# Optimization experiments

Measured on AMD Instinct MI355X. Metric: run time of the kernel, lower is better.

Reference implementation:

```python
import jax, jax.numpy as jnp
import numpy as np

N_NODES = 20000
N_EDGES = 320000
F_IN = 64      # num_node_features
C = 64         # out_features (per-head channels, concat=False)
H = 4          # n_heads
L = 3          # n_layers (stackable since F_IN == C)
N_RES = 2
N_PAIRS = 8192
EDGE_DIM = 9
HID = 64 * C   # ResNetGated hidden dim = 64 * out_features
N_EXPERTS = 8


def setup_inputs() -> dict:
    key = jax.random.key(0)
    ks = jax.random.split(key, 24)
    s = 0.05
    f32 = jnp.float32
    inp = {}
    inp["x"] = jax.random.normal(ks[0], (N_NODES, F_IN), f32)
    inp["edge_index"] = jax.random.randint(ks[1], (2, N_EDGES), 0, N_NODES)
    inp["edge_attr"] = jax.random.normal(ks[2], (N_EDGES, EDGE_DIM), f32)
    inp["edge_cross"] = jax.random.randint(ks[3], (N_PAIRS, 2), 0, N_NODES)
    inp["types"] = jax.random.randint(ks[4], (N_PAIRS,), 0, N_EXPERTS)
    # GATv2 encoder params, stacked over L layers (layer 0 in-dim == C)
    inp["gat_Wl"] = jax.random.normal(ks[5], (L, F_IN, H * C), f32) * s
    inp["gat_bl"] = jnp.full((L, H * C), 0.01, f32)
    inp["gat_Wr"] = jax.random.normal(ks[6], (L, F_IN, H * C), f32) * s
    inp["gat_br"] = jnp.full((L, H * C), 0.01, f32)
    inp["gat_We"] = jax.random.normal(ks[7], (L, EDGE_DIM, H * C), f32) * s  # lin_edge, no bias
    inp["gat_att"] = jax.random.normal(ks[8], (L, H, C), f32) * s
    inp["gat_bias"] = jnp.zeros((L, C), f32)
    inp["gat_gates"] = jax.random.normal(ks[9], (L,), f32) * 0.5
    # 8 type-routed experts: ResNetGated(2C -> 64C -> 2C) x N_RES, then Linear(2C, 1)
    inp["res_W1"] = jax.random.normal(ks[10], (N_EXPERTS, N_RES, 2 * C, HID), f32) * s
    inp["res_b1"] = jnp.full((N_EXPERTS, N_RES, HID), 0.01, f32)
    inp["res_W2"] = jax.random.normal(ks[11], (N_EXPERTS, N_RES, HID, 2 * C), f32) * s
    inp["res_b2"] = jnp.full((N_EXPERTS, N_RES, 2 * C), 0.01, f32)
    inp["res_gates"] = jax.random.normal(ks[12], (N_EXPERTS, N_RES), f32) * 0.5
    inp["head_W"] = jax.random.normal(ks[13], (N_EXPERTS, 2 * C, 1), f32) * s
    inp["head_b"] = jnp.full((N_EXPERTS, 1), 0.01, f32)
    return inp


def _gat_layer(h, src, tgt, ea, Wl, bl, Wr, br, We, att, bias):
    # GATv2Conv with edge features, concat=False (mean over heads)
    n = h.shape[0]
    nh, c = att.shape
    xl = (h @ Wl + bl).reshape(n, nh, c)   # source transform (x_j)
    xr = (h @ Wr + br).reshape(n, nh, c)   # target transform (x_i)
    e = (ea @ We).reshape(-1, nh, c)
    m = jax.nn.leaky_relu(xl[src] + xr[tgt] + e, 0.2)       # [E,H,C]
    logits = jnp.einsum('ehc,hc->eh', m, att)               # [E,H]
    mx = jax.ops.segment_max(logits, tgt, num_segments=n)
    a = jnp.exp(logits - mx[tgt])
    den = jax.ops.segment_sum(a, tgt, num_segments=n)
    alpha = a / den[tgt]                                     # segment softmax over in-edges
    out = jax.ops.segment_sum(xl[src] * alpha[:, :, None], tgt, num_segments=n)
    return out.mean(axis=1) + bias


def reference(x, edge_index, edge_attr, edge_cross, types,
              gat_Wl, gat_bl, gat_Wr, gat_br, gat_We, gat_att, gat_bias, gat_gates,
              res_W1, res_b1, res_W2, res_b2, res_gates, head_W, head_b):
    src, tgt = edge_index[0], edge_index[1]
    g = jax.nn.sigmoid(gat_gates)
    h = _gat_layer(x, src, tgt, edge_attr, gat_Wl[0], gat_bl[0], gat_Wr[0], gat_br[0],
                   gat_We[0], gat_att[0], gat_bias[0])
    for i in range(1, gat_Wl.shape[0]):
        h = jax.nn.leaky_relu(h, 0.01)
        hi = _gat_layer(h, src, tgt, edge_attr, gat_Wl[i], gat_bl[i], gat_Wr[i], gat_br[i],
                        gat_We[i], gat_att[i], gat_bias[i])
        h = g[i - 1] * hi + (1 - g[i - 1]) * h
    # pair gather + feature interleave: x[edge_cross].transpose(1,2).reshape(P, 2C)
    pair = h[edge_cross]                               # [P,2,C]
    p = pair.shape[0]
    z0 = jnp.swapaxes(pair, 1, 2).reshape(p, -1)        # [P,2C]
    outs = []
    for e in range(res_W1.shape[0]):
        z = z0
        ge = jax.nn.sigmoid(res_gates[e])
        for r in range(res_W1.shape[1]):
            z = jax.nn.relu(z)
            y = jax.nn.relu(z @ res_W1[e, r] + res_b1[e, r]) @ res_W2[e, r] + res_b2[e, r]
            z = ge[r] * y + (1 - ge[r]) * z
        outs.append(z @ head_W[e] + head_b[e])          # [P,1]
    all_out = jnp.stack(outs)                           # [8,P,1]
    per_row = all_out[types, jnp.arange(p)]             # [P,1] per-row expert output
    order = jnp.argsort(types, stable=True)             # concat groups type 0..7, stable in-group
    return per_row[order]
```

## Files before the change

### kernel.cpp

```cpp
#include <hip/hip_runtime.h>

#define NN 20000
#define NE 320000
#define NL 3
#define NP 8192
#define EDIM 9
#define TROWS 32
#define MAXT 272
#define CAPR (MAXT*TROWS)
#define NB ((NN+255)/256)

typedef _Float16 f16x8 __attribute__((ext_vector_type(8)));
typedef float f32x4 __attribute__((ext_vector_type(4)));

#define GLL16(g,l) __builtin_amdgcn_global_load_lds((const __attribute__((address_space(1))) unsigned int*)(g), (__attribute__((address_space(3))) unsigned int*)(l), 16, 0, 0)

__device__ __forceinline__ float sigm(float x){ return 1.f/(1.f+__expf(-x)); }

__device__ __forceinline__ float dpp_sum64(float x){
  x += __int_as_float(__builtin_amdgcn_update_dpp(0, __float_as_int(x), 0x111, 0xf, 0xf, true));
  x += __int_as_float(__builtin_amdgcn_update_dpp(0, __float_as_int(x), 0x112, 0xf, 0xf, true));
  x += __int_as_float(__builtin_amdgcn_update_dpp(0, __float_as_int(x), 0x114, 0xf, 0xf, true));
  x += __int_as_float(__builtin_amdgcn_update_dpp(0, __float_as_int(x), 0x118, 0xf, 0xf, true));
  x += __int_as_float(__builtin_amdgcn_update_dpp(0, __float_as_int(x), 0x142, 0xf, 0xf, true));
  x += __int_as_float(__builtin_amdgcn_update_dpp(0, __float_as_int(x), 0x143, 0xf, 0xf, true));
  return __uint_as_float(__builtin_amdgcn_readlane(__float_as_uint(x), 63));
}

__global__ void k_deg(const int* __restrict__ ei, int* __restrict__ deg){
  int e=blockIdx.x*blockDim.x+threadIdx.x; if(e<NE) atomicAdd(&deg[ei[NE+e]],1);
}

__global__ __launch_bounds__(256) void k_scan1(const int* __restrict__ deg, int* __restrict__ incl, int* __restrict__ bsum){
  __shared__ int sh[256];
  int b=blockIdx.x, tid=threadIdx.x;
  int i=b*256+tid;
  int v=(i<NN)?deg[i]:0;
  sh[tid]=v; __syncthreads();
  for(int o=1;o<256;o<<=1){
    int t=(tid>=o)?sh[tid-o]:0; __syncthreads();
    sh[tid]+=t; __syncthreads();
  }
  if(i<NN) incl[i]=sh[tid];
  if(tid==255) bsum[b]=sh[255];
}
__global__ __launch_bounds__(256) void k_scan3(const int* __restrict__ deg, const int* __restrict__ incl,
                        const int* __restrict__ bsum, int* __restrict__ row_ptr, int* __restrict__ cursor){
  __shared__ int sh[256];
  int b=blockIdx.x, tid=threadIdx.x;
  sh[tid]=(tid<b && tid<NB)?bsum[tid]:0;
  __syncthreads();
  for(int o=128;o>0;o>>=1){ if(tid<o) sh[tid]+=sh[tid+o]; __syncthreads(); }
  int boff=sh[0];
  int i=b*256+tid;
  if(i<NN){
    int r=incl[i]+boff;
    row_ptr[i+1]=r; cursor[i]=r-deg[i];
  }
  if(i==0) row_ptr[0]=0;
}

__global__ void k_fill_csr2(const int* __restrict__ ei, const float* __restrict__ ea,
    int* __restrict__ cursor, int* __restrict__ csr_src, float* __restrict__ eas){
  int e=blockIdx.x*blockDim.x+threadIdx.x;
  if(e<NE){
    int t=ei[NE+e]; int pos=atomicAdd(&cursor[t],1);
    csr_src[pos]=ei[e];
    const float* s=ea+(size_t)e*9;
    float* d=eas+(size_t)pos*12;
    #pragma unroll
    for(int k=0;k<9;++k) d[k]=s[k];
    d[9]=0.f; d[10]=0.f; d[11]=0.f;
  }
}

__global__ __launch_bounds__(256) void k_sort(const int* __restrict__ types, int* __restrict__ meta,
    int* __restrict__ slotp, int* __restrict__ islot){
  __shared__ int cnt[256][8];
  __shared__ int tot[8];
  __shared__ int base_s[8], pad_s[8];
  int tid=threadIdx.x;
  int lc[8]={0,0,0,0,0,0,0,0};
  int tl[32];
  for(int i=0;i<32;++i){ int ty=types[tid*32+i]; tl[i]=ty; lc[ty]++; }
  #pragma unroll
  for(int t=0;t<8;++t) cnt[tid][t]=lc[t];
  __syncthreads();
  if(tid<8){
    int run=0;
    for(int j=0;j<256;++j){ int v=cnt[j][tid]; cnt[j][tid]=run; run+=v; }
    tot[tid]=run;
  }
  __syncthreads();
  if(tid==0){
    int b=0, pb=0, nt=0;
    for(int t=0;t<8;++t){
      base_s[t]=b; pad_s[t]=pb;
      meta[t]=tot[t]; meta[8+t]=b; meta[16+t]=pb;
      int ntt=(tot[t]+31)>>5;
      for(int j=0;j<ntt;++j){ meta[32+nt]=t; meta[32+MAXT+nt]=pb+j*32; nt++; }
      b+=tot[t]; pb+=ntt*32;
    }
    meta[24]=nt; meta[25]=pb;
  }
  __syncthreads();
  if(tid<8){
    int t=tid; int ntt=(tot[t]+31)>>5;
    for(int sr=tot[t]; sr<ntt*32; ++sr) islot[pad_s[t]+sr]=-1;
  }
  int run[8];
  #pragma unroll
  for(int t=0;t<8;++t) run[t]=cnt[tid][t];
  for(int i=0;i<32;++i){
    int p=tid*32+i; int t=tl[i]; int r=run[t]++;
    int pos=base_s[t]+r, slot=pad_s[t]+r;
    slotp[p]=slot; islot[slot]=pos;
  }
}

__global__ __launch_bounds__(256) void k_nodexf(const float* __restrict__ hin,
    const float* __restrict__ Wl, const float* __restrict__ bl,
    const float* __restrict__ Wr, const float* __restrict__ br,
    float* __restrict__ xl, float* __restrict__ xr, int lk){
  __shared__ float hsT[64][68];
  __shared__ float ws[64][68];
  int bid=blockIdx.x;
  int n0=(bid>>3)*64, ch=bid&7;
  const float* W=(ch<4)?Wl:Wr;
  const float* bb=(ch<4)?bl:br;
  float* outp=(ch<4)?xl:xr;
  int c0=(ch&3)*64;
  int tid=threadIdx.x;

  for(int idx=tid; idx<64*16; idx+=256){
    int r=idx&63, kq=idx>>6;
    int n=n0+r;
    float4 v=make_float4(0.f,0.f,0.f,0.f);
    if(n<NN) v=*(const float4*)&hin[(size_t)n*64+kq*4];
    if(lk){
      v.x=v.x>0.f?v.x:0.01f*v.x; v.y=v.y>0.f?v.y:0.01f*v.y;
      v.z=v.z>0.f?v.z:0.01f*v.z; v.w=v.w>0.f?v.w:0.01f*v.w;
    }
    hsT[kq*4+0][r]=v.x; hsT[kq*4+1][r]=v.y; hsT[kq*4+2][r]=v.z; hsT[kq*4+3][r]=v.w;
  }
  for(int idx=tid; idx<64*16; idx+=256){
    int k=idx>>4, j4=idx&15;
    *(float4*)&ws[k][j4*4]=*(const float4*)&W[(size_t)k*256+c0+j4*4];
  }
  __syncthreads();

  int ty=tid>>4, tx=tid&15;
  float acc[4][4]={};
  #pragma unroll 4
  for(int k=0;k<64;++k){
    float4 a=*(const float4*)&hsT[k][4*ty];
    float4 b=*(const float4*)&ws[k][4*tx];
    float aa[4]={a.x,a.y,a.z,a.w}, bbv[4]={b.x,b.y,b.z,b.w};
    #pragma unroll
    for(int i=0;i<4;++i){
      #pragma unroll
      for(int j=0;j<4;++j) acc[i][j]=fmaf(aa[i],bbv[j],acc[i][j]);
    }
  }
  float4 bias4=*(const float4*)&bb[c0+4*tx];
  #pragma unroll
  for(int i=0;i<4;++i){
    int n=n0+4*ty+i;
    if(n<NN){
      float4 o=make_float4(acc[i][0]+bias4.x, acc[i][1]+bias4.y, acc[i][2]+bias4.z, acc[i][3]+bias4.w);
      *(float4*)&outp[(size_t)n*256+c0+4*tx]=o;
    }
  }
}

__global__ __launch_bounds__(256) void k_agg2(const float* __restrict__ xl, const float* __restrict__ xr,
    const float* __restrict__ eas, const int* __restrict__ csr_src, const int* __restrict__ row_ptr,
    const float* __restrict__ WeL, const float* __restrict__ attL,
    const float* __restrict__ biasL, const float* __restrict__ gates, int layer,
    const float* __restrict__ hprev, float* __restrict__ hout){
  __shared__ float red[4][64];
  int n=blockIdx.x, tid=threadIdx.x;
  float w0=WeL[tid],      w1=WeL[256+tid],  w2=WeL[512+tid],  w3=WeL[768+tid],  w4=WeL[1024+tid];
  float w5=WeL[1280+tid], w6=WeL[1536+tid], w7=WeL[1792+tid], w8=WeL[2048+tid];
  float att_t=attL[tid];
  float xr_t=xr[(size_t)n*256+tid];
  int s=row_ptr[n], t=row_ptr[n+1];
  float den=0.f, acc=0.f;

  auto body=[&](float xlv, int j){
    const float4* ep=(const float4*)(eas+(size_t)j*12);
    float4 e0=ep[0], e1=ep[1];
    float e8=eas[(size_t)j*12+8];
    float ev=e0.x*w0+e0.y*w1+e0.z*w2+e0.w*w3+e1.x*w4+e1.y*w5+e1.z*w6+e1.w*w7+e8*w8;
    float m=xlv+xr_t+ev;
    m=m>0.f?m:0.2f*m;
    float pt=dpp_sum64(m*att_t);
    float a=__expf(pt);
    den+=a; acc+=a*xlv;
  };

  float x0=0.f,x1=0.f,x2=0.f,x3=0.f;
  if(s+0<t) x0=xl[(size_t)csr_src[s+0]*256+tid];
  if(s+1<t) x1=xl[(size_t)csr_src[s+1]*256+tid];
  if(s+2<t) x2=xl[(size_t)csr_src[s+2]*256+tid];
  if(s+3<t) x3=xl[(size_t)csr_src[s+3]*256+tid];
  int j=s;
  while(j+7<t){
    float y0=xl[(size_t)csr_src[j+4]*256+tid];
    float y1=xl[(size_t)csr_src[j+5]*256+tid];
    float y2=xl[(size_t)csr_src[j+6]*256+tid];
    float y3=xl[(size_t)csr_src[j+7]*256+tid];
    body(x0,j); body(x1,j+1); body(x2,j+2); body(x3,j+3);
    x0=y0; x1=y1; x2=y2; x3=y3;
    j+=4;
  }
  if(j<t){ body(x0,j); ++j; }
  if(j<t){ body(x1,j); ++j; }
  if(j<t){ body(x2,j); ++j; }
  if(j<t){ body(x3,j); ++j; }
  while(j<t){ body(xl[(size_t)csr_src[j]*256+tid], j); ++j; }

  float rdn=den>0.f?1.f/den:0.f;
  int h=tid>>6, cc=tid&63;
  red[h][cc]=acc*rdn;
  __syncthreads();
  if(tid<64){
    float mean=(red[0][tid]+red[1][tid]+red[2][tid]+red[3][tid])*0.25f + biasL[tid];
    float o;
    if(layer==0) o=mean;
    else{
      float hp=hprev[(size_t)n*64+tid];
      hp=hp>0.f?hp:0.01f*hp;
      float g=sigm(gates[layer-1]);
      o=g*mean+(1.f-g)*hp;
    }
    hout[(size_t)n*64+tid]=o;
  }
}

__global__ __launch_bounds__(256) void k_prep_all(const float* __restrict__ rW1, _Float16* __restrict__ w1t,
    const float* __restrict__ rW2, _Float16* __restrict__ w2t,
    const float* __restrict__ hfin, const int* __restrict__ ecross,
    const int* __restrict__ slotp, float* __restrict__ z){
  __shared__ float lds[128*33];
  int bigbid=blockIdx.x, tid=threadIdx.x;
  if(bigbid<2048){
    int bid=bigbid, er=bid>>7, ch=bid&127;
    const float* s=rW1+(size_t)er*128*4096 + ch*32;
    for(int idx=tid; idx<128*32; idx+=256){ int k=idx>>5, jl=idx&31; lds[k*33+jl]=s[(size_t)k*4096+jl]; }
    __syncthreads();
    _Float16* d=w1t+(size_t)bid*4096;
    for(int g=tid; g<512; g+=256){
      int jl=g>>4, k8=g&15;
      f16x8 v;
      #pragma unroll
      for(int t=0;t<8;++t) v[t]=(_Float16)lds[(k8*8+t)*33+jl];
      int elem=(jl*128+k8*8)^((jl&7)<<3);
      *(f16x8*)(&d[elem])=v;
    }
  }else if(bigbid<4096){
    int bid=bigbid-2048, er=bid>>7, ch=bid&127;
    const float* s=rW2+(size_t)er*4096*128 + (size_t)ch*32*128;
    for(int idx=tid; idx<32*128; idx+=256){ int j=idx>>7, n=idx&127; lds[j*130+n]=s[(size_t)j*128+n]; }
    __syncthreads();
    _Float16* d=w2t+(size_t)bid*4096;
    for(int g=tid; g<512; g+=256){
      int n=g>>2, j8=g&3;
      f16x8 v;
      #pragma unroll
      for(int t=0;t<8;++t) v[t]=(_Float16)lds[(j8*8+t)*130+n];
      int elem=(n*32+j8*8)^((n&7)<<3);
      *(f16x8*)(&d[elem])=v;
    }
  }else{
    int g=(bigbid-4096)*256+tid;
    int p=g>>6, c=g&63;
    int a=ecross[2*p], b=ecross[2*p+1];
    int slot=slotp[p];
    float2 v; v.x=hfin[(size_t)a*64+c]; v.y=hfin[(size_t)b*64+c];
    ((float2*)(z+(size_t)slot*128))[c]=v;
  }
}

__global__ __launch_bounds__(256) void k_resmfma(const float* __restrict__ zin,
    const _Float16* __restrict__ w1t, const _Float16* __restrict__ w2t,
    const float* __restrict__ b1all, const int* __restrict__ meta,
    float* __restrict__ ypart, int rb)
{
  __shared__ _Float16 wb[2][8192];
  __shared__ _Float16 ts[2][32*32];
  __shared__ float b1s[1024];
  int bidl=blockIdx.x;
  int bid=(bidl&7)*132+(bidl>>3);
  int v=bid>>2, hq=bid&3;
  int nt=meta[24];
  if(v>=nt) return;
  int e=meta[32+v], row0=meta[32+MAXT+v];
  int er=e*2+rb;
  const _Float16* w1b=w1t+(size_t)er*524288 + (size_t)hq*32*4096;
  const _Float16* w2b=w2t+(size_t)er*524288 + (size_t)hq*32*4096;
  const float* b1g=b1all+(size_t)er*4096 + hq*1024;
  int tid=threadIdx.x, l=tid&63, w=tid>>6;
  int lm=l&15, lq=l>>4;
  int s16=(w&1)*16, jh=w>>1;
  int arow=s16+lm;

  f16x8 af[4];
  {
    const float* zr=zin+(size_t)(row0+arow)*128;
    #pragma unroll
    for(int ks=0;ks<4;++ks){
      const float* src=zr+ks*32+lq*8;
      float4 v0=*(const float4*)src;
      float4 v1=*(const float4*)(src+4);
      f16x8 hv;
      hv[0]=(_Float16)fmaxf(v0.x,0.f); hv[1]=(_Float16)fmaxf(v0.y,0.f);
      hv[2]=(_Float16)fmaxf(v0.z,0.f); hv[3]=(_Float16)fmaxf(v0.w,0.f);
      hv[4]=(_Float16)fmaxf(v1.x,0.f); hv[5]=(_Float16)fmaxf(v1.y,0.f);
      hv[6]=(_Float16)fmaxf(v1.z,0.f); hv[7]=(_Float16)fmaxf(v1.w,0.f);
      af[ks]=hv;
    }
  }
  for(int g=tid; g<1024; g+=256) b1s[g]=b1g[g];

  #pragma unroll
  for(int s=0;s<2;++s){
    int so=(w*2+s)*512;
    GLL16(w1b+so+l*8, &wb[0][so]);
    GLL16(w2b+so+l*8, &wb[0][4096+so]);
  }
  asm volatile("s_waitcnt lgkmcnt(0)" ::: "memory");
  __builtin_amdgcn_sched_barrier(0);
  __builtin_amdgcn_s_barrier();

  f32x4 yacc[4];
  #pragma unroll
  for(int i=0;i<4;++i){ yacc[i][0]=0.f; yacc[i][1]=0.f; yacc[i][2]=0.f; yacc[i][3]=0.f; }

  for(int cc=0; cc<32; ++cc){
    int buf=cc&1;
    asm volatile("s_waitcnt vmcnt(0)" ::: "memory");
    __builtin_amdgcn_sched_barrier(0);
    __builtin_amdgcn_s_barrier();
    if(cc<31){
      const _Float16* g1=w1b+(size_t)(cc+1)*4096;
      const _Float16* g2=w2b+(size_t)(cc+1)*4096;
      int nb=buf^1;
      #pragma unroll
      for(int s=0;s<2;++s){
        int so=(w*2+s)*512;
        GLL16(g1+so+l*8, &wb[nb][so]);
        GLL16(g2+so+l*8, &wb[nb][4096+so]);
      }
    }

    f32x4 tacc={0.f,0.f,0.f,0.f};
    int j=jh*16+lm;
    #pragma unroll
    for(int ks=0;ks<4;++ks){
      f16x8 b=*(const f16x8*)(&wb[buf][(j*128+ks*32+lq*8)^((j&7)<<3)]);
      tacc=__builtin_amdgcn_mfma_f32_16x16x32_f16(af[ks],b,tacc,0,0,0);
    }
    float b1v=b1s[cc*32+j];
    int tbuf=cc&1;
    #pragma unroll
    for(int r=0;r<4;++r){
      int trow=s16+lq*4+r;
      ts[tbuf][(trow*32+j)^((trow&7)<<3)]=(_Float16)fmaxf(tacc[r]+b1v,0.f);
    }
    asm volatile("s_waitcnt lgkmcnt(0)" ::: "memory");
    __builtin_amdgcn_sched_barrier(0);
    __builtin_amdgcn_s_barrier();

    f16x8 a2=*(const f16x8*)(&ts[tbuf][(arow*32+lq*8)^((arow&7)<<3)]);
    #pragma unroll
    for(int nf=0;nf<4;++nf){
      int n=jh*64+nf*16+lm;
      f16x8 b=*(const f16x8*)(&wb[buf][4096+((n*32+lq*8)^((n&7)<<3))]);
      yacc[nf]=__builtin_amdgcn_mfma_f32_16x16x32_f16(a2,b,yacc[nf],0,0,0);
    }
  }

  float* yp=ypart+(size_t)hq*CAPR*128;
  #pragma unroll
  for(int nf=0;nf<4;++nf){
    int col=jh*64+nf*16+lm;
    #pragma unroll
    for(int r=0;r<4;++r)
      yp[(size_t)(row0+s16+lq*4+r)*128+col]=yacc[nf][r];
  }
}

__global__ __launch_bounds__(256) void k_comb(const float* __restrict__ zin, const float* __restrict__ ypart,
    const float* __restrict__ b2all, const float* __restrict__ gates, const int* __restrict__ meta,
    int rb, float* __restrict__ zout,
    const float* __restrict__ hWg, const float* __restrict__ hbg, const int* __restrict__ islot,
    float* __restrict__ out)
{
  int v=blockIdx.x;
  if(v>=meta[24]) return;
  int e=meta[32+v], row0=meta[32+MAXT+v];
  int er=e*2+rb;
  float ge=sigm(gates[er]);
  const float* b2=b2all+(size_t)er*128;
  int tid=threadIdx.x;
  const size_t HS=(size_t)CAPR*128;
  if(rb==0){
    for(int idx=tid; idx<32*128; idx+=256){
      int r=idx>>7, c=idx&127;
      size_t o=(size_t)(row0+r)*128+c;
      float y=ypart[o]+ypart[HS+o]+ypart[2*HS+o]+ypart[3*HS+o];
      float zr=fmaxf(zin[o],0.f);
      zout[o]=ge*(y+b2[c])+(1.f-ge)*zr;
    }
  }else{
    int r=tid>>3, cs=tid&7;
    float acc=0.f;
    size_t ro=(size_t)(row0+r)*128;
    #pragma unroll
    for(int q=0;q<16;++q){
      int c=cs*16+q;
      size_t o=ro+c;
      float y=ypart[o]+ypart[HS+o]+ypart[2*HS+o]+ypart[3*HS+o];
      float zr=fmaxf(zin[o],0.f);
      float zf=ge*(y+b2[c])+(1.f-ge)*zr;
      acc+=zf*hWg[e*128+c];
    }
    acc+=__shfl_xor(acc,1); acc+=__shfl_xor(acc,2); acc+=__shfl_xor(acc,4);
    if(cs==0){
      int pos=islot[row0+r];
      if(pos>=0) out[pos]=acc+hbg[e];
    }
  }
}

extern "C" void kernel_launch(void* const* d_in, const int* in_sizes, int n_in,
                              void* d_out, int out_size, void* d_ws, size_t ws_size,
                              hipStream_t stream){
  const float* x     =(const float*)d_in[0];
  const int*   ei    =(const int*)  d_in[1];
  const float* ea    =(const float*)d_in[2];
  const int*   ecross=(const int*)  d_in[3];
  const int*   types =(const int*)  d_in[4];
  const float* gWl   =(const float*)d_in[5];
  const float* gbl   =(const float*)d_in[6];
  const float* gWr   =(const float*)d_in[7];
  const float* gbr   =(const float*)d_in[8];
  const float* gWe   =(const float*)d_in[9];
  const float* gatt  =(const float*)d_in[10];
  const float* gbias =(const float*)d_in[11];
  const float* ggate =(const float*)d_in[12];
  const float* rW1   =(const float*)d_in[13];
  const float* rb1   =(const float*)d_in[14];
  const float* rW2   =(const float*)d_in[15];
  const float* rb2   =(const float*)d_in[16];
  const float* rg    =(const float*)d_in[17];
  const float* hW    =(const float*)d_in[18];
  const float* hb    =(const float*)d_in[19];
  float* out=(float*)d_out;

  char* base=(char*)d_ws;
  size_t off=0;
  auto alloc=[&](size_t bytes)->char*{
    char* p=base+off;
    off=(off+bytes+511)&~((size_t)511);
    return p;
  };
  float* hA     =(float*)alloc((size_t)NN*64*4);
  float* hB     =(float*)alloc((size_t)NN*64*4);
  int*   deg    =(int*)  alloc((size_t)NN*4);
  int*   row_ptr=(int*)  alloc((size_t)(NN+1)*4);
  int*   cursor =(int*)  alloc((size_t)NN*4);
  int*   incl   =(int*)  alloc((size_t)NN*4);
  int*   bsum   =(int*)  alloc(256*4);
  int*   csr_src=(int*)  alloc((size_t)(NE+16)*4);
  int*   meta   =(int*)  alloc(1024*4);
  int*   slotp  =(int*)  alloc((size_t)NP*4);
  int*   islot  =(int*)  alloc((size_t)CAPR*4);
  float* zA     =(float*)alloc((size_t)CAPR*128*4);
  size_t uoff=off;
  float* xl =(float*)(base+uoff);
  float* xr =(float*)(base+uoff+(size_t)NN*256*4);
  float* eas=(float*)(base+uoff+(size_t)NN*256*4*2);
  _Float16* w1t=(_Float16*)(base+uoff);
  _Float16* w2t=(_Float16*)(base+uoff+(size_t)16*524288*2);
  float* ypart =(float*)(base+uoff+(size_t)16*524288*2*2);
  size_t gat_bytes=(size_t)NN*256*4*2 + (size_t)(NE*12+16)*4;
  size_t exp_bytes=(size_t)16*524288*2*2 + (size_t)4*CAPR*128*4;
  size_t need=uoff+(gat_bytes>exp_bytes?gat_bytes:exp_bytes);
  if(ws_size<need) return;
  float* zB=hB;

  hipMemsetAsync(deg,0,(size_t)NN*4,stream);
  k_deg<<<(NE+255)/256,256,0,stream>>>(ei,deg);
  k_scan1<<<NB,256,0,stream>>>(deg,incl,bsum);
  k_scan3<<<NB,256,0,stream>>>(deg,incl,bsum,row_ptr,cursor);
  k_fill_csr2<<<(NE+255)/256,256,0,stream>>>(ei,ea,cursor,csr_src,eas);
  k_sort<<<1,256,0,stream>>>(types,meta,slotp,islot);

  const float* hcur=x;
  float* hnext=hA;
  for(int L=0;L<NL;++L){
    k_nodexf<<<((NN+63)/64)*8,256,0,stream>>>(hcur, gWl+(size_t)L*64*256, gbl+(size_t)L*256,
                                              gWr+(size_t)L*64*256, gbr+(size_t)L*256, xl, xr, L>0?1:0);
    k_agg2<<<NN,256,0,stream>>>(xl,xr,eas,csr_src,row_ptr, gWe+(size_t)L*EDIM*256,
                                gatt+(size_t)L*256, gbias+(size_t)L*64, ggate, L, hcur, hnext);
    hcur=hnext;
    hnext=(hcur==hA)?hB:hA;
  }

  k_prep_all<<<6144,256,0,stream>>>(rW1,w1t,rW2,w2t,hcur,ecross,slotp,zA);

  k_resmfma<<<1056,256,0,stream>>>(zA,w1t,w2t,rb1,meta,ypart,0);
  k_comb<<<MAXT,256,0,stream>>>(zA,ypart,rb2,rg,meta,0,zB,hW,hb,islot,out);
  k_resmfma<<<1056,256,0,stream>>>(zB,w1t,w2t,rb1,meta,ypart,1);
  k_comb<<<MAXT,256,0,stream>>>(zB,ypart,rb2,rg,meta,1,zA,hW,hb,islot,out);

  (void)in_sizes; (void)n_in; (void)out_size;
}
```

Before: 555.4 us.

## Split GAT edge aggregation across wavefronts with float4 per-lane channels

The GATv2 aggregation kernel is restructured so each of the four wavefronts in a block walks a strided quarter of the node's incoming edges. Each lane handles four channels of one head through float4 loads, and each head's attention logit is reduced with a 16-lane DPP all-sum instead of a full 64-lane reduction plus readlane. Partial numerators and denominators from the four wavefronts are combined in shared memory at the end. This cuts the serial per-edge dependency chain and the reduction cost per edge, in exchange for more registers and an extra LDS combine. The softmax still uses no max subtraction, as before.

```diff
diff --git a/kernel.cpp b/kernel.cpp
--- a/kernel.cpp
+++ b/kernel.cpp
@@ -17,14 +17,22 @@
 
 __device__ __forceinline__ float sigm(float x){ return 1.f/(1.f+__expf(-x)); }
 
-__device__ __forceinline__ float dpp_sum64(float x){
-  x += __int_as_float(__builtin_amdgcn_update_dpp(0, __float_as_int(x), 0x111, 0xf, 0xf, true));
-  x += __int_as_float(__builtin_amdgcn_update_dpp(0, __float_as_int(x), 0x112, 0xf, 0xf, true));
-  x += __int_as_float(__builtin_amdgcn_update_dpp(0, __float_as_int(x), 0x114, 0xf, 0xf, true));
-  x += __int_as_float(__builtin_amdgcn_update_dpp(0, __float_as_int(x), 0x118, 0xf, 0xf, true));
-  x += __int_as_float(__builtin_amdgcn_update_dpp(0, __float_as_int(x), 0x142, 0xf, 0xf, true));
-  x += __int_as_float(__builtin_amdgcn_update_dpp(0, __float_as_int(x), 0x143, 0xf, 0xf, true));
-  return __uint_as_float(__builtin_amdgcn_readlane(__float_as_uint(x), 63));
+template<int CTRL>
+__device__ __forceinline__ float dpp_mov(float x){
+  return __int_as_float(__builtin_amdgcn_update_dpp(0, __float_as_int(x), CTRL, 0xf, 0xf, true));
+}
+__device__ __forceinline__ float row_allsum16(float x, int l){
+  x += dpp_mov<0xB1>(x);
+  x += dpp_mov<0x4E>(x);
+  float a4=dpp_mov<0x104>(x), b4=dpp_mov<0x114>(x);
+  x += (l&4)? b4 : a4;
+  float a8=dpp_mov<0x108>(x), b8=dpp_mov<0x118>(x);
+  x += (l&8)? b8 : a8;
+  return x;
+}
+
+__device__ __forceinline__ float4 f4fma(float s, float4 a, float4 b){
+  return make_float4(fmaf(s,a.x,b.x), fmaf(s,a.y,b.y), fmaf(s,a.z,b.z), fmaf(s,a.w,b.w));
 }
 
 __global__ void k_deg(const int* __restrict__ ei, int* __restrict__ deg){
@@ -173,68 +181,89 @@
   }
 }
 
-__global__ __launch_bounds__(256) void k_agg2(const float* __restrict__ xl, const float* __restrict__ xr,
+__global__ __launch_bounds__(256) void k_agg5(const float* __restrict__ xl, const float* __restrict__ xr,
     const float* __restrict__ eas, const int* __restrict__ csr_src, const int* __restrict__ row_ptr,
     const float* __restrict__ WeL, const float* __restrict__ attL,
     const float* __restrict__ biasL, const float* __restrict__ gates, int layer,
     const float* __restrict__ hprev, float* __restrict__ hout){
-  __shared__ float red[4][64];
-  int n=blockIdx.x, tid=threadIdx.x;
-  float w0=WeL[tid],      w1=WeL[256+tid],  w2=WeL[512+tid],  w3=WeL[768+tid],  w4=WeL[1024+tid];
-  float w5=WeL[1280+tid], w6=WeL[1536+tid], w7=WeL[1792+tid], w8=WeL[2048+tid];
-  float att_t=attL[tid];
-  float xr_t=xr[(size_t)n*256+tid];
+  __shared__ float racc[4][256];
+  __shared__ float rden[4][4];
+  int n=blockIdx.x, tid=threadIdx.x, w=tid>>6, l=tid&63;
+  int h=l>>4, cg=l&15;
+  int ch0=h*64+cg*4;
+  float4 Wk[9];
+  #pragma unroll
+  for(int k=0;k<9;++k) Wk[k]=*(const float4*)&WeL[k*256+ch0];
+  float4 att=*(const float4*)&attL[ch0];
+  float4 xr4=*(const float4*)&xr[(size_t)n*256+ch0];
   int s=row_ptr[n], t=row_ptr[n+1];
-  float den=0.f, acc=0.f;
-
-  auto body=[&](float xlv, int j){
-    const float4* ep=(const float4*)(eas+(size_t)j*12);
-    float4 e0=ep[0], e1=ep[1];
-    float e8=eas[(size_t)j*12+8];
-    float ev=e0.x*w0+e0.y*w1+e0.z*w2+e0.w*w3+e1.x*w4+e1.y*w5+e1.z*w6+e1.w*w7+e8*w8;
-    float m=xlv+xr_t+ev;
-    m=m>0.f?m:0.2f*m;
-    float pt=dpp_sum64(m*att_t);
+  float den=0.f;
+  float4 acc=make_float4(0.f,0.f,0.f,0.f);
+
+  auto body=[&](float4 xc, int j){
+    const float* ej=eas+(size_t)j*12;
+    float4 e0=*(const float4*)ej;
+    float4 e1=*(const float4*)(ej+4);
+    float e8=ej[8];
+    float4 m=make_float4(xc.x+xr4.x, xc.y+xr4.y, xc.z+xr4.z, xc.w+xr4.w);
+    m=f4fma(e0.x,Wk[0],m); m=f4fma(e0.y,Wk[1],m); m=f4fma(e0.z,Wk[2],m);
+    m=f4fma(e0.w,Wk[3],m); m=f4fma(e1.x,Wk[4],m); m=f4fma(e1.y,Wk[5],m);
+    m=f4fma(e1.z,Wk[6],m); m=f4fma(e1.w,Wk[7],m); m=f4fma(e8 ,Wk[8],m);
+    m.x=fmaxf(m.x,0.f)+0.2f*fminf(m.x,0.f);
+    m.y=fmaxf(m.y,0.f)+0.2f*fminf(m.y,0.f);
+    m.z=fmaxf(m.z,0.f)+0.2f*fminf(m.z,0.f);
+    m.w=fmaxf(m.w,0.f)+0.2f*fminf(m.w,0.f);
+    float pl=fmaf(m.x,att.x, fmaf(m.y,att.y, fmaf(m.z,att.z, m.w*att.w)));
+    float pt=row_allsum16(pl,l);
     float a=__expf(pt);
-    den+=a; acc+=a*xlv;
+    den+=a;
+    acc=f4fma(a,xc,acc);
   };
 
-  float x0=0.f,x1=0.f,x2=0.f,x3=0.f;
-  if(s+0<t) x0=xl[(size_t)csr_src[s+0]*256+tid];
-  if(s+1<t) x1=xl[(size_t)csr_src[s+1]*256+tid];
-  if(s+2<t) x2=xl[(size_t)csr_src[s+2]*256+tid];
-  if(s+3<t) x3=xl[(size_t)csr_src[s+3]*256+tid];
-  int j=s;
-  while(j+7<t){
-    float y0=xl[(size_t)csr_src[j+4]*256+tid];
-    float y1=xl[(size_t)csr_src[j+5]*256+tid];
-    float y2=xl[(size_t)csr_src[j+6]*256+tid];
-    float y3=xl[(size_t)csr_src[j+7]*256+tid];
-    body(x0,j); body(x1,j+1); body(x2,j+2); body(x3,j+3);
+  int j=s+w;
+  float4 z4=make_float4(0.f,0.f,0.f,0.f);
+  float4 x0=z4,x1=z4,x2=z4,x3=z4;
+  if(j   <t) x0=*(const float4*)&xl[(size_t)csr_src[j   ]*256+ch0];
+  if(j+4 <t) x1=*(const float4*)&xl[(size_t)csr_src[j+4 ]*256+ch0];
+  if(j+8 <t) x2=*(const float4*)&xl[(size_t)csr_src[j+8 ]*256+ch0];
+  if(j+12<t) x3=*(const float4*)&xl[(size_t)csr_src[j+12]*256+ch0];
+  while(j+28<t){
+    float4 y0=*(const float4*)&xl[(size_t)csr_src[j+16]*256+ch0];
+    float4 y1=*(const float4*)&xl[(size_t)csr_src[j+20]*256+ch0];
+    float4 y2=*(const float4*)&xl[(size_t)csr_src[j+24]*256+ch0];
+    float4 y3=*(const float4*)&xl[(size_t)csr_src[j+28]*256+ch0];
+    body(x0,j); body(x1,j+4); body(x2,j+8); body(x3,j+12);
     x0=y0; x1=y1; x2=y2; x3=y3;
-    j+=4;
-  }
-  if(j<t){ body(x0,j); ++j; }
-  if(j<t){ body(x1,j); ++j; }
-  if(j<t){ body(x2,j); ++j; }
-  if(j<t){ body(x3,j); ++j; }
-  while(j<t){ body(xl[(size_t)csr_src[j]*256+tid], j); ++j; }
-
-  float rdn=den>0.f?1.f/den:0.f;
-  int h=tid>>6, cc=tid&63;
-  red[h][cc]=acc*rdn;
+    j+=16;
+  }
+  if(j<t){ body(x0,j); j+=4; }
+  if(j<t){ body(x1,j); j+=4; }
+  if(j<t){ body(x2,j); j+=4; }
+  if(j<t){ body(x3,j); j+=4; }
+  while(j<t){ body(*(const float4*)&xl[(size_t)csr_src[j]*256+ch0], j); j+=4; }
+
+  *(float4*)&racc[w][ch0]=acc;
+  if(cg==0) rden[w][h]=den;
   __syncthreads();
   if(tid<64){
-    float mean=(red[0][tid]+red[1][tid]+red[2][tid]+red[3][tid])*0.25f + biasL[tid];
-    float o;
-    if(layer==0) o=mean;
+    int c=tid;
+    float o=0.f;
+    #pragma unroll
+    for(int h2=0;h2<4;++h2){
+      float av=racc[0][h2*64+c]+racc[1][h2*64+c]+racc[2][h2*64+c]+racc[3][h2*64+c];
+      float dv=rden[0][h2]+rden[1][h2]+rden[2][h2]+rden[3][h2];
+      o += dv>0.f ? av/dv : 0.f;
+    }
+    float mean=o*0.25f + biasL[c];
+    float ov;
+    if(layer==0) ov=mean;
     else{
-      float hp=hprev[(size_t)n*64+tid];
+      float hp=hprev[(size_t)n*64+c];
       hp=hp>0.f?hp:0.01f*hp;
       float g=sigm(gates[layer-1]);
-      o=g*mean+(1.f-g)*hp;
-    }
-    hout[(size_t)n*64+tid]=o;
+      ov=g*mean+(1.f-g)*hp;
+    }
+    hout[(size_t)n*64+c]=ov;
   }
 }
 
@@ -503,7 +532,7 @@
   for(int L=0;L<NL;++L){
     k_nodexf<<<((NN+63)/64)*8,256,0,stream>>>(hcur, gWl+(size_t)L*64*256, gbl+(size_t)L*256,
                                               gWr+(size_t)L*64*256, gbr+(size_t)L*256, xl, xr, L>0?1:0);
-    k_agg2<<<NN,256,0,stream>>>(xl,xr,eas,csr_src,row_ptr, gWe+(size_t)L*EDIM*256,
+    k_agg5<<<NN,256,0,stream>>>(xl,xr,eas,csr_src,row_ptr, gWe+(size_t)L*EDIM*256,
                                 gatt+(size_t)L*256, gbias+(size_t)L*64, ggate, L, hcur, hnext);
     hcur=hnext;
     hnext=(hcur==hA)?hB:hA;
```

New measurement: 628.9 us. 1.13x slower.
